# Performance work log

Measured on AMD Instinct MI355X. Metric: run time of the kernel, lower is better.

The kernel has to match this reference:

```python
import jax, jax.numpy as jnp
import numpy as np


def gcn_conv(x, src, dst, W, b, N):
    """PyG GCNConv: add self-loops, symmetric D^-1/2 (A+I) D^-1/2 normalization."""
    loop = jnp.arange(N, dtype=src.dtype)
    s = jnp.concatenate([src, loop])
    d = jnp.concatenate([dst, loop])
    deg = jnp.zeros((N,), dtype=x.dtype).at[d].add(1.0)  # in-degree incl. self-loop
    dinv = jax.lax.rsqrt(deg)  # deg >= 1 because of self-loops
    norm = dinv[s] * dinv[d]  # [E+N]
    h = x @ W  # [N, out] linear transform first (as in PyG)
    msg = h[s] * norm[:, None]  # gather + scale
    out = jax.ops.segment_sum(msg, d, num_segments=N)  # scatter-add
    return out + b


def setup_inputs() -> dict:
    key = jax.random.key(0)
    ks = jax.random.split(key, 10)
    N, E, in_dim, h1, h2, A = 100000, 3200000, 256, 32, 64, 64
    x = jax.random.normal(ks[0], (N, in_dim), dtype=jnp.float32)
    ei = jax.random.randint(ks[1], (2, E), 0, N, dtype=jnp.int64)
    def glorot(k, shape):
        lim = float(np.sqrt(6.0 / (shape[0] + shape[1])))
        return jax.random.uniform(k, shape, jnp.float32, -lim, lim)
    return {
        "x": x,
        "ei": ei,
        "num_nodes": N,
        "W1": glorot(ks[2], (in_dim, h1)), "b1": jnp.zeros((h1,), jnp.float32),
        "W2": glorot(ks[3], (h1, h2)),     "b2": jnp.zeros((h2,), jnp.float32),
        "Wo1": glorot(ks[4], (h2, h2)),    "bo1": jnp.zeros((h2,), jnp.float32),
        "Wo2": glorot(ks[5], (h2, A)),     "bo2": jnp.zeros((A,), jnp.float32),
    }


def reference(x, ei, num_nodes, W1, b1, W2, b2, Wo1, bo1, Wo2, bo2):
    src, dst = ei[0], ei[1]
    z = jax.nn.relu(gcn_conv(x, src, dst, W1, b1, num_nodes))
    z = jax.nn.relu(gcn_conv(z, src, dst, W2, b2, num_nodes))
    logits = jax.nn.relu(z @ Wo1 + bo1) @ Wo2 + bo2  # [N, action_space]
    nbatches = z.shape[0] // num_nodes
    # original reshapes with z.size(1)=hidden2 (== action_space here)
    dist = logits.reshape(nbatches, num_nodes * z.shape[1])
    return jax.nn.softmax(dist, axis=-1)  # Categorical probs
```

## Files before the change

kernel.cpp:

```cpp
#include <hip/hip_runtime.h>

#define DEVI __device__ __forceinline__

DEVI unsigned fkey(float f) {
  unsigned u = __float_as_uint(f);
  return u ^ ((u >> 31) ? 0xFFFFFFFFu : 0x80000000u);
}
DEVI float funkey(unsigned k) {
  unsigned b = (k & 0x80000000u) ? (k ^ 0x80000000u) : ~k;
  return __uint_as_float(b);
}
DEVI float f4get(const float4& v, int j) {
  return j == 0 ? v.x : j == 1 ? v.y : j == 2 ? v.z : v.w;
}

constexpr int BSH = 9;
constexpr int BNODES = 1 << BSH;
constexpr int PEPT = 16;
constexpr int PCHUNK = 256 * PEPT;

__global__ void k_binit(int* __restrict__ bcnt) {
  bcnt[threadIdx.x] = 0;
}

__global__ void k_bcount(const int* __restrict__ dst, int* __restrict__ bcnt,
                         int E, int NB) {
  __shared__ int lh[256];
  lh[threadIdx.x] = 0;
  __syncthreads();
  int stride = gridDim.x * 256;
  for (long i = (long)blockIdx.x * 256 + threadIdx.x; i < E; i += stride)
    atomicAdd(&lh[dst[i] >> BSH], 1);
  __syncthreads();
  if (threadIdx.x < NB && lh[threadIdx.x]) atomicAdd(&bcnt[threadIdx.x], lh[threadIdx.x]);
}

__global__ void k_bscan(const int* __restrict__ bcnt, int* __restrict__ bbase,
                        int* __restrict__ bcur, unsigned* __restrict__ scal, int NB) {
  __shared__ int s[256];
  int t = threadIdx.x;
  int v = (t < NB) ? bcnt[t] : 0;
  s[t] = v;
  __syncthreads();
  for (int o = 1; o < 256; o <<= 1) {
    int add = (t >= o) ? s[t - o] : 0;
    __syncthreads();
    s[t] += add;
    __syncthreads();
  }
  int excl = s[t] - v;
  if (t < NB) { bbase[t] = excl; bcur[t] = excl; }
  if (t == 0) { scal[0] = 0u; scal[1] = 0u; }
}

__global__ __launch_bounds__(256)
void k_bpart(const int* __restrict__ src, const int* __restrict__ dst,
             int* __restrict__ bcur, unsigned* __restrict__ epart, int E, int NB) {
  __shared__ int lh[256];
  __shared__ int gbase[256];
  long base = (long)blockIdx.x * PCHUNK;
  lh[threadIdx.x] = 0;
  __syncthreads();
  int ed[PEPT]; int es[PEPT]; unsigned short lpos[PEPT];
#pragma unroll
  for (int j = 0; j < PEPT; j++) {
    long i = base + threadIdx.x + (long)j * 256;
    if (i < E) {
      int d = dst[i];
      es[j] = src[i];
      ed[j] = d;
      lpos[j] = (unsigned short)atomicAdd(&lh[d >> BSH], 1);
    } else {
      ed[j] = -1;
    }
  }
  __syncthreads();
  if (threadIdx.x < NB) {
    int c = lh[threadIdx.x];
    gbase[threadIdx.x] = c ? atomicAdd(&bcur[threadIdx.x], c) : 0;
  }
  __syncthreads();
#pragma unroll
  for (int j = 0; j < PEPT; j++) {
    int d = ed[j];
    if (d >= 0) {
      unsigned p = (unsigned)(gbase[d >> BSH] + (int)lpos[j]);
      epart[p] = ((unsigned)(d & (BNODES - 1)) << 17) | (unsigned)es[j];
    }
  }
}

__global__ __launch_bounds__(256)
void k_fine(const unsigned* __restrict__ epart, const int* __restrict__ bbase,
            const int* __restrict__ bcnt, int* __restrict__ rowptr,
            int* __restrict__ deg, float* __restrict__ dinv,
            int* __restrict__ col, int N) {
  __shared__ int lh[BNODES];
  __shared__ int lexcl[BNODES];
  __shared__ int ssc[256];
  int b = blockIdx.x;
  int base = bbase[b], cnt = bcnt[b];
  int nlo = b << BSH;
  int t = threadIdx.x;
  lh[t] = 0; lh[t + 256] = 0;
  __syncthreads();
  for (int i = t; i < cnt; i += 256) {
    unsigned e = epart[base + i];
    atomicAdd(&lh[e >> 17], 1);
  }
  __syncthreads();
  int a0 = lh[2 * t], a1 = lh[2 * t + 1];
  ssc[t] = a0 + a1;
  __syncthreads();
  for (int o = 1; o < 256; o <<= 1) {
    int add = (t >= o) ? ssc[t - o] : 0;
    __syncthreads();
    ssc[t] += add;
    __syncthreads();
  }
  int excl = ssc[t] - (a0 + a1);
  lexcl[2 * t] = excl;
  lexcl[2 * t + 1] = excl + a0;
  __syncthreads();
#pragma unroll
  for (int k = 0; k < 2; k++) {
    int i = t + k * 256;
    int v = nlo + i;
    if (v < N) {
      int dgv = lh[i];
      deg[v] = dgv;
      rowptr[v] = base + lexcl[i];
      dinv[v] = rsqrtf((float)(dgv + 1));
    }
  }
  __syncthreads();
  lh[2 * t] = lexcl[2 * t];
  lh[2 * t + 1] = lexcl[2 * t + 1];
  __syncthreads();
  for (int i = t; i < cnt; i += 256) {
    unsigned e = epart[base + i];
    int p = atomicAdd(&lh[e >> 17], 1);
    col[base + p] = (int)(e & 0x1FFFFu);
  }
}

__global__ __launch_bounds__(256)
void k_gemm1(const float* __restrict__ in, const float* __restrict__ W,
             const float* __restrict__ dinv, float* __restrict__ out, int N) {
  __shared__ float Wl[256 * 32];
  __shared__ float xb[2][128 * 16];
  const int t = threadIdx.x;

  {
    const float4* W4 = (const float4*)W;
    float4* Wl4 = (float4*)Wl;
#pragma unroll
    for (int i = 0; i < 8; i++) Wl4[t + i * 256] = W4[t + i * 256];
  }

  const int srow = t >> 1;
  const int part = t & 1;
  const int sk = (srow >> 1) & 3;
  long grow = (long)blockIdx.x * 128 + srow;
  const float* gsrc = in + (grow < (long)N ? grow : (long)(N - 1)) * 256 + part * 8;
  const int q0 = part * 2, q1 = part * 2 + 1;
  const int ws0 = srow * 16 + ((q0 ^ sk) << 2);
  const int ws1 = srow * 16 + ((q1 ^ sk) << 2);

  const int cg = t & 3;
  const int rg = t >> 2;
  const int c0 = cg * 8;
  const int rk = (rg >> 1) & 3;

  {
    float4 a = *(const float4*)(gsrc + 0);
    float4 b = *(const float4*)(gsrc + 4);
    *(float4*)&xb[0][ws0] = a;
    *(float4*)&xb[0][ws1] = b;
  }
  __syncthreads();

  float acc[2][8];
#pragma unroll
  for (int i = 0; i < 2; i++)
#pragma unroll
    for (int c = 0; c < 8; c++) acc[i][c] = 0.f;

  for (int ch = 0; ch < 16; ch++) {
    float4 na, nb;
    if (ch < 15) {
      na = *(const float4*)(gsrc + (ch + 1) * 16 + 0);
      nb = *(const float4*)(gsrc + (ch + 1) * 16 + 4);
    }
    const float* xc = xb[ch & 1];
#pragma unroll
    for (int q = 0; q < 4; q++) {
      float4 xv0 = *(const float4*)&xc[rg * 16 + ((q ^ rk) << 2)];
      float4 xv1 = *(const float4*)&xc[(rg + 64) * 16 + ((q ^ rk) << 2)];
#pragma unroll
      for (int jj = 0; jj < 4; jj++) {
        const float* wr = &Wl[(ch * 16 + q * 4 + jj) * 32 + c0];
        float4 wa = *(const float4*)(wr);
        float4 wb = *(const float4*)(wr + 4);
        float x0 = f4get(xv0, jj);
        float x1 = f4get(xv1, jj);
        acc[0][0] = fmaf(x0, wa.x, acc[0][0]);
        acc[0][1] = fmaf(x0, wa.y, acc[0][1]);
        acc[0][2] = fmaf(x0, wa.z, acc[0][2]);
        acc[0][3] = fmaf(x0, wa.w, acc[0][3]);
        acc[0][4] = fmaf(x0, wb.x, acc[0][4]);
        acc[0][5] = fmaf(x0, wb.y, acc[0][5]);
        acc[0][6] = fmaf(x0, wb.z, acc[0][6]);
        acc[0][7] = fmaf(x0, wb.w, acc[0][7]);
        acc[1][0] = fmaf(x1, wa.x, acc[1][0]);
        acc[1][1] = fmaf(x1, wa.y, acc[1][1]);
        acc[1][2] = fmaf(x1, wa.z, acc[1][2]);
        acc[1][3] = fmaf(x1, wa.w, acc[1][3]);
        acc[1][4] = fmaf(x1, wb.x, acc[1][4]);
        acc[1][5] = fmaf(x1, wb.y, acc[1][5]);
        acc[1][6] = fmaf(x1, wb.z, acc[1][6]);
        acc[1][7] = fmaf(x1, wb.w, acc[1][7]);
      }
    }
    if (ch < 15) {
      __syncthreads();
      float* xn = xb[(ch + 1) & 1];
      *(float4*)&xn[ws0] = na;
      *(float4*)&xn[ws1] = nb;
      __syncthreads();
    }
  }

#pragma unroll
  for (int i = 0; i < 2; i++) {
    long r = (long)blockIdx.x * 128 + rg + i * 64;
    if (r < (long)N) {
      float dv = dinv[r];
      float* op = &out[r * 32 + c0];
      *(float4*)(op) = make_float4(acc[i][0] * dv, acc[i][1] * dv,
                                   acc[i][2] * dv, acc[i][3] * dv);
      *(float4*)(op + 4) = make_float4(acc[i][4] * dv, acc[i][5] * dv,
                                       acc[i][6] * dv, acc[i][7] * dv);
    }
  }
}

__global__ __launch_bounds__(256)
void k_head(const float* __restrict__ s2,
            const float* __restrict__ W2, const float* __restrict__ b2,
            const float* __restrict__ Wo1, const float* __restrict__ bo1,
            const float* __restrict__ Wo2, const float* __restrict__ bo2,
            float* __restrict__ out, int N, unsigned* __restrict__ gmax) {
  __shared__ float A[64 * 64];
  __shared__ float B[64 * 64];
  __shared__ float xr[128 * 64];
  const int t = threadIdx.x;
  const int cg = t & 7, rg = t >> 3;
  const int c0 = cg * 8;
  const int key = rg & 7;
  const long r0 = (long)blockIdx.x * 128 + rg * 4;

  {
    const float4* w2 = (const float4*)W2;
    const float4* w1 = (const float4*)Wo1;
    float4* Af = (float4*)A;
    float4* Bf = (float4*)B;
    Af[t] = w2[t];
    Af[t + 256] = w2[t + 256];
#pragma unroll
    for (int i = 0; i < 4; i++) Bf[t + i * 256] = w1[t + i * 256];
  }
  __syncthreads();

  bool rv[4];
  int xrow[4];
#pragma unroll
  for (int i = 0; i < 4; i++) {
    rv[i] = (r0 + i) < (long)N;
    xrow[i] = (rg + 32 * i) * 64;
  }

  float acc[4][8];

#pragma unroll
  for (int i = 0; i < 4; i++)
#pragma unroll
    for (int c = 0; c < 8; c++) acc[i][c] = 0.f;
  {
    const float* ip = s2 + r0 * 32;
#pragma unroll 2
    for (int k = 0; k < 32; k += 4) {
      float4 xv[4];
#pragma unroll
      for (int i = 0; i < 4; i++)
        xv[i] = rv[i] ? *(const float4*)(ip + i * 32 + k)
                      : make_float4(0.f, 0.f, 0.f, 0.f);
#pragma unroll
      for (int jj = 0; jj < 4; jj++) {
        float4 wa = *(const float4*)&A[(k + jj) * 64 + c0];
        float4 wb = *(const float4*)&A[(k + jj) * 64 + c0 + 4];
#pragma unroll
        for (int i = 0; i < 4; i++) {
          float xs = f4get(xv[i], jj);
          acc[i][0] = fmaf(xs, wa.x, acc[i][0]);
          acc[i][1] = fmaf(xs, wa.y, acc[i][1]);
          acc[i][2] = fmaf(xs, wa.z, acc[i][2]);
          acc[i][3] = fmaf(xs, wa.w, acc[i][3]);
          acc[i][4] = fmaf(xs, wb.x, acc[i][4]);
          acc[i][5] = fmaf(xs, wb.y, acc[i][5]);
          acc[i][6] = fmaf(xs, wb.z, acc[i][6]);
          acc[i][7] = fmaf(xs, wb.w, acc[i][7]);
        }
      }
    }
    float bo[8];
#pragma unroll
    for (int c = 0; c < 8; c++) bo[c] = b2[c0 + c];
    const int q0 = (2 * cg) ^ key, q1 = (2 * cg + 1) ^ key;
#pragma unroll
    for (int i = 0; i < 4; i++) {
      float v0 = fmaxf(acc[i][0] + bo[0], 0.f);
      float v1 = fmaxf(acc[i][1] + bo[1], 0.f);
      float v2 = fmaxf(acc[i][2] + bo[2], 0.f);
      float v3 = fmaxf(acc[i][3] + bo[3], 0.f);
      float v4 = fmaxf(acc[i][4] + bo[4], 0.f);
      float v5 = fmaxf(acc[i][5] + bo[5], 0.f);
      float v6 = fmaxf(acc[i][6] + bo[6], 0.f);
      float v7 = fmaxf(acc[i][7] + bo[7], 0.f);
      *(float4*)&xr[xrow[i] + 4 * q0] = make_float4(v0, v1, v2, v3);
      *(float4*)&xr[xrow[i] + 4 * q1] = make_float4(v4, v5, v6, v7);
    }
  }
  __syncthreads();

  float4 wo2r[4];
  {
    const float4* w = (const float4*)Wo2;
#pragma unroll
    for (int i = 0; i < 4; i++) wo2r[i] = w[t + i * 256];
  }

#pragma unroll
  for (int i = 0; i < 4; i++)
#pragma unroll
    for (int c = 0; c < 8; c++) acc[i][c] = 0.f;
#pragma unroll 2
  for (int k = 0; k < 64; k += 4) {
    const int q = k >> 2;
    float4 xv[4];
#pragma unroll
    for (int i = 0; i < 4; i++)
      xv[i] = *(const float4*)&xr[xrow[i] + 4 * (q ^ key)];
#pragma unroll
    for (int jj = 0; jj < 4; jj++) {
      float4 wa = *(const float4*)&B[(k + jj) * 64 + c0];
      float4 wb = *(const float4*)&B[(k + jj) * 64 + c0 + 4];
#pragma unroll
      for (int i = 0; i < 4; i++) {
        float xs = f4get(xv[i], jj);
        acc[i][0] = fmaf(xs, wa.x, acc[i][0]);
        acc[i][1] = fmaf(xs, wa.y, acc[i][1]);
        acc[i][2] = fmaf(xs, wa.z, acc[i][2]);
        acc[i][3] = fmaf(xs, wa.w, acc[i][3]);
        acc[i][4] = fmaf(xs, wb.x, acc[i][4]);
        acc[i][5] = fmaf(xs, wb.y, acc[i][5]);
        acc[i][6] = fmaf(xs, wb.z, acc[i][6]);
        acc[i][7] = fmaf(xs, wb.w, acc[i][7]);
      }
    }
  }
  __syncthreads();

  {
    float4* Af = (float4*)A;
#pragma unroll
    for (int i = 0; i < 4; i++) Af[t + i * 256] = wo2r[i];
    float bo[8];
#pragma unroll
    for (int c = 0; c < 8; c++) bo[c] = bo1[c0 + c];
    const int q0 = (2 * cg) ^ key, q1 = (2 * cg + 1) ^ key;
#pragma unroll
    for (int i = 0; i < 4; i++) {
      float v0 = fmaxf(acc[i][0] + bo[0], 0.f);
      float v1 = fmaxf(acc[i][1] + bo[1], 0.f);
      float v2 = fmaxf(acc[i][2] + bo[2], 0.f);
      float v3 = fmaxf(acc[i][3] + bo[3], 0.f);
      float v4 = fmaxf(acc[i][4] + bo[4], 0.f);
      float v5 = fmaxf(acc[i][5] + bo[5], 0.f);
      float v6 = fmaxf(acc[i][6] + bo[6], 0.f);
      float v7 = fmaxf(acc[i][7] + bo[7], 0.f);
      *(float4*)&xr[xrow[i] + 4 * q0] = make_float4(v0, v1, v2, v3);
      *(float4*)&xr[xrow[i] + 4 * q1] = make_float4(v4, v5, v6, v7);
    }
  }
  __syncthreads();

#pragma unroll
  for (int i = 0; i < 4; i++)
#pragma unroll
    for (int c = 0; c < 8; c++) acc[i][c] = 0.f;
#pragma unroll 2
  for (int k = 0; k < 64; k += 4) {
    const int q = k >> 2;
    float4 xv[4];
#pragma unroll
    for (int i = 0; i < 4; i++)
      xv[i] = *(const float4*)&xr[xrow[i] + 4 * (q ^ key)];
#pragma unroll
    for (int jj = 0; jj < 4; jj++) {
      float4 wa = *(const float4*)&A[(k + jj) * 64 + c0];
      float4 wb = *(const float4*)&A[(k + jj) * 64 + c0 + 4];
#pragma unroll
      for (int i = 0; i < 4; i++) {
        float xs = f4get(xv[i], jj);
        acc[i][0] = fmaf(xs, wa.x, acc[i][0]);
        acc[i][1] = fmaf(xs, wa.y, acc[i][1]);
        acc[i][2] = fmaf(xs, wa.z, acc[i][2]);
        acc[i][3] = fmaf(xs, wa.w, acc[i][3]);
        acc[i][4] = fmaf(xs, wb.x, acc[i][4]);
        acc[i][5] = fmaf(xs, wb.y, acc[i][5]);
        acc[i][6] = fmaf(xs, wb.z, acc[i][6]);
        acc[i][7] = fmaf(xs, wb.w, acc[i][7]);
      }
    }
  }
  float m = -3.4e38f;
  {
    float bo[8];
#pragma unroll
    for (int c = 0; c < 8; c++) bo[c] = bo2[c0 + c];
#pragma unroll
    for (int i = 0; i < 4; i++) {
      if (!rv[i]) continue;
      float o[8];
#pragma unroll
      for (int c = 0; c < 8; c++) {
        float v = acc[i][c] + bo[c];
        m = fmaxf(m, v);
        o[c] = v;
      }
      float* op = &out[(r0 + i) * 64 + c0];
      *(float4*)(op) = make_float4(o[0], o[1], o[2], o[3]);
      *(float4*)(op + 4) = make_float4(o[4], o[5], o[6], o[7]);
    }
  }
  __syncthreads();
  xr[t] = m;
  __syncthreads();
  for (int o2 = 128; o2 > 0; o2 >>= 1) {
    if (t < o2) xr[t] = fmaxf(xr[t], xr[t + o2]);
    __syncthreads();
  }
  if (t == 0) atomicMax(gmax, fkey(xr[0]));
}

template <int FEAT, bool BIAS, bool RELU, bool PSCALE>
__launch_bounds__(256)
__global__ void k_aggv(const float* __restrict__ g, const int* __restrict__ col,
                       const int* __restrict__ rowptr, const int* __restrict__ deg,
                       const float* __restrict__ dinv, const float* __restrict__ bias,
                       float* __restrict__ out, int N) {
  constexpr int LPN = FEAT / 4;
  constexpr int NPB = 256 / LPN;
  int nib = threadIdx.x / LPN;
  int c = threadIdx.x % LPN;
  long v = (long)blockIdx.x * NPB + nib;
  if (v >= N) return;

  const float4* g4 = (const float4*)g;
  float4 acc = g4[v * LPN + c];
  int start = rowptr[v], dg = deg[v];
  int e = 0;
  while (e < dg) {
    int cnt = min(LPN, dg - e);
    int idx = (c < cnt) ? col[start + e + c] : 0;
    int j = 0;
    for (; j + 4 <= cnt; j += 4) {
      int u0 = __shfl(idx, j + 0, LPN);
      int u1 = __shfl(idx, j + 1, LPN);
      int u2 = __shfl(idx, j + 2, LPN);
      int u3 = __shfl(idx, j + 3, LPN);
      float4 a0 = g4[(long)u0 * LPN + c];
      float4 a1 = g4[(long)u1 * LPN + c];
      float4 a2 = g4[(long)u2 * LPN + c];
      float4 a3 = g4[(long)u3 * LPN + c];
      acc.x += (a0.x + a1.x) + (a2.x + a3.x);
      acc.y += (a0.y + a1.y) + (a2.y + a3.y);
      acc.z += (a0.z + a1.z) + (a2.z + a3.z);
      acc.w += (a0.w + a1.w) + (a2.w + a3.w);
    }
    for (; j < cnt; j++) {
      int u = __shfl(idx, j, LPN);
      float4 a = g4[(long)u * LPN + c];
      acc.x += a.x; acc.y += a.y; acc.z += a.z; acc.w += a.w;
    }
    e += cnt;
  }
  float dv = dinv[v];
  float4 val;
  val.x = acc.x * dv; val.y = acc.y * dv; val.z = acc.z * dv; val.w = acc.w * dv;
  if (BIAS) {
    float4 b = ((const float4*)bias)[c];
    val.x += b.x; val.y += b.y; val.z += b.z; val.w += b.w;
  }
  if (RELU) {
    val.x = fmaxf(val.x, 0.f); val.y = fmaxf(val.y, 0.f);
    val.z = fmaxf(val.z, 0.f); val.w = fmaxf(val.w, 0.f);
  }
  if (PSCALE) {
    val.x *= dv; val.y *= dv; val.z *= dv; val.w *= dv;
  }
  ((float4*)out)[v * LPN + c] = val;
}

__global__ void k_smsum(const float* __restrict__ logit, unsigned* __restrict__ scal, int total) {
  __shared__ float s[256];
  float gmax = funkey(scal[0]);
  float loc = 0.f;
  for (int i = blockIdx.x * 256 + threadIdx.x; i < total; i += gridDim.x * 256)
    loc += expf(logit[i] - gmax);
  s[threadIdx.x] = loc; __syncthreads();
  for (int o = 128; o > 0; o >>= 1) {
    if (threadIdx.x < o) s[threadIdx.x] += s[threadIdx.x + o];
    __syncthreads();
  }
  if (threadIdx.x == 0) atomicAdd((float*)&scal[1], s[0]);
}

__global__ void k_smnorm(float* __restrict__ logit, const unsigned* __restrict__ scal, int total) {
  float gmax = funkey(scal[0]);
  float inv = 1.0f / __uint_as_float(scal[1]);
  int i = blockIdx.x * 256 + threadIdx.x;
  if (i < total) logit[i] = expf(logit[i] - gmax) * inv;
}

extern "C" void kernel_launch(void* const* d_in, const int* in_sizes, int n_in,
                              void* d_out, int out_size, void* d_ws, size_t ws_size,
                              hipStream_t stream) {
  const float* x   = (const float*)d_in[0];
  const int*   ei  = (const int*)d_in[1];
  const float* W1  = (const float*)d_in[3];
  const float* b1  = (const float*)d_in[4];
  const float* W2  = (const float*)d_in[5];
  const float* b2  = (const float*)d_in[6];
  const float* Wo1 = (const float*)d_in[7];
  const float* bo1 = (const float*)d_in[8];
  const float* Wo2 = (const float*)d_in[9];
  const float* bo2 = (const float*)d_in[10];

  const int N = in_sizes[0] / 256;
  const int E = in_sizes[1] / 2;
  const int* src = ei;
  const int* dst = ei + E;
  const int NB = (N + BNODES - 1) / BNODES;

  size_t o = 0;
  auto carve = [&](size_t bytes) -> char* {
    char* p = (char*)d_ws + o;
    o += (bytes + 255) & ~(size_t)255;
    return p;
  };
  float* R1     = (float*)carve((size_t)N * 64 * 4);
  float* R2     = (float*)carve((size_t)N * 64 * 4);
  int*   col    = (int*)carve((size_t)E * 4);
  int*   deg    = (int*)carve((size_t)N * 4);
  float* dinv   = (float*)carve((size_t)N * 4);
  int*   rowptr = (int*)carve((size_t)N * 4);
  int*   bcnt   = (int*)carve(256 * 4);
  int*   bbase  = (int*)carve(256 * 4);
  int*   bcur   = (int*)carve(256 * 4);
  unsigned* scal = (unsigned*)carve(64);

  unsigned* epart = (unsigned*)R2;
  float* g1 = R1;
  float* p  = R2;
  float* s2 = R1;
  float* logits = (float*)d_out;

  k_binit<<<1, 256, 0, stream>>>(bcnt);
  k_bcount<<<512, 256, 0, stream>>>(dst, bcnt, E, NB);
  k_bscan<<<1, 256, 0, stream>>>(bcnt, bbase, bcur, scal, NB);
  k_bpart<<<(E + PCHUNK - 1) / PCHUNK, 256, 0, stream>>>(src, dst, bcur, epart, E, NB);
  k_fine<<<NB, 256, 0, stream>>>(epart, bbase, bcnt, rowptr, deg, dinv, col, N);

  const int g1G = (N + 127) / 128;
  const int gA = (N + 31) / 32;

  k_gemm1<<<g1G, 256, 0, stream>>>(x, W1, dinv, g1, N);
  k_aggv<32, true, true, true><<<gA, 256, 0, stream>>>(g1, col, rowptr, deg, dinv, b1, p, N);

  k_aggv<32, false, false, false><<<gA, 256, 0, stream>>>(p, col, rowptr, deg, dinv, nullptr, s2, N);

  k_head<<<g1G, 256, 0, stream>>>(s2, W2, b2, Wo1, bo1, Wo2, bo2, logits, N, scal);

  k_smsum<<<1024, 256, 0, stream>>>(logits, scal, out_size);
  k_smnorm<<<(out_size + 255) / 256, 256, 0, stream>>>(logits, scal, out_size);
}
```

Baseline: 495.9 us.

## Keep head MLP activations in registers and exchange via shuffles instead of LDS

The fused head kernel no longer stages intermediate activations through a large shared-memory tile. Each group of 8 lanes exchanges its row's activation values with width-8 shuffles, and only one 16KB weight buffer is kept, reloaded between layers. The block max reduction becomes a wavefront shuffle reduction with one atomic per wave rather than a tree over shared memory. This cuts LDS use sharply, which should allow more resident blocks, at the cost of many extra shuffle instructions and more register pressure.

```diff
diff --git a/kernel.cpp b/kernel.cpp
--- a/kernel.cpp
+++ b/kernel.cpp
@@ -252,40 +252,35 @@
             const float* __restrict__ Wo2, const float* __restrict__ bo2,
             float* __restrict__ out, int N, unsigned* __restrict__ gmax) {
   __shared__ float A[64 * 64];
-  __shared__ float B[64 * 64];
-  __shared__ float xr[128 * 64];
   const int t = threadIdx.x;
   const int cg = t & 7, rg = t >> 3;
   const int c0 = cg * 8;
-  const int key = rg & 7;
   const long r0 = (long)blockIdx.x * 128 + rg * 4;
 
   {
     const float4* w2 = (const float4*)W2;
-    const float4* w1 = (const float4*)Wo1;
     float4* Af = (float4*)A;
-    float4* Bf = (float4*)B;
     Af[t] = w2[t];
     Af[t + 256] = w2[t + 256];
-#pragma unroll
-    for (int i = 0; i < 4; i++) Bf[t + i * 256] = w1[t + i * 256];
+  }
+  float4 wn[4];
+  {
+    const float4* w = (const float4*)Wo1;
+#pragma unroll
+    for (int i = 0; i < 4; i++) wn[i] = w[t + i * 256];
   }
   __syncthreads();
 
   bool rv[4];
-  int xrow[4];
-#pragma unroll
-  for (int i = 0; i < 4; i++) {
-    rv[i] = (r0 + i) < (long)N;
-    xrow[i] = (rg + 32 * i) * 64;
-  }
-
-  float acc[4][8];
+#pragma unroll
+  for (int i = 0; i < 4; i++) rv[i] = (r0 + i) < (long)N;
+
+  float a1[4][8], a2[4][8];
 
 #pragma unroll
   for (int i = 0; i < 4; i++)
 #pragma unroll
-    for (int c = 0; c < 8; c++) acc[i][c] = 0.f;
+    for (int c = 0; c < 8; c++) a1[i][c] = 0.f;
   {
     const float* ip = s2 + r0 * 32;
 #pragma unroll 2
@@ -302,128 +297,122 @@
 #pragma unroll
         for (int i = 0; i < 4; i++) {
           float xs = f4get(xv[i], jj);
-          acc[i][0] = fmaf(xs, wa.x, acc[i][0]);
-          acc[i][1] = fmaf(xs, wa.y, acc[i][1]);
-          acc[i][2] = fmaf(xs, wa.z, acc[i][2]);
-          acc[i][3] = fmaf(xs, wa.w, acc[i][3]);
-          acc[i][4] = fmaf(xs, wb.x, acc[i][4]);
-          acc[i][5] = fmaf(xs, wb.y, acc[i][5]);
-          acc[i][6] = fmaf(xs, wb.z, acc[i][6]);
-          acc[i][7] = fmaf(xs, wb.w, acc[i][7]);
+          a1[i][0] = fmaf(xs, wa.x, a1[i][0]);
+          a1[i][1] = fmaf(xs, wa.y, a1[i][1]);
+          a1[i][2] = fmaf(xs, wa.z, a1[i][2]);
+          a1[i][3] = fmaf(xs, wa.w, a1[i][3]);
+          a1[i][4] = fmaf(xs, wb.x, a1[i][4]);
+          a1[i][5] = fmaf(xs, wb.y, a1[i][5]);
+          a1[i][6] = fmaf(xs, wb.z, a1[i][6]);
+          a1[i][7] = fmaf(xs, wb.w, a1[i][7]);
         }
       }
     }
     float bo[8];
 #pragma unroll
     for (int c = 0; c < 8; c++) bo[c] = b2[c0 + c];
-    const int q0 = (2 * cg) ^ key, q1 = (2 * cg + 1) ^ key;
-#pragma unroll
-    for (int i = 0; i < 4; i++) {
-      float v0 = fmaxf(acc[i][0] + bo[0], 0.f);
-      float v1 = fmaxf(acc[i][1] + bo[1], 0.f);
-      float v2 = fmaxf(acc[i][2] + bo[2], 0.f);
-      float v3 = fmaxf(acc[i][3] + bo[3], 0.f);
-      float v4 = fmaxf(acc[i][4] + bo[4], 0.f);
-      float v5 = fmaxf(acc[i][5] + bo[5], 0.f);
-      float v6 = fmaxf(acc[i][6] + bo[6], 0.f);
-      float v7 = fmaxf(acc[i][7] + bo[7], 0.f);
-      *(float4*)&xr[xrow[i] + 4 * q0] = make_float4(v0, v1, v2, v3);
-      *(float4*)&xr[xrow[i] + 4 * q1] = make_float4(v4, v5, v6, v7);
-    }
-  }
-  __syncthreads();
-
-  float4 wo2r[4];
-  {
+#pragma unroll
+    for (int i = 0; i < 4; i++)
+#pragma unroll
+      for (int c = 0; c < 8; c++) a1[i][c] = fmaxf(a1[i][c] + bo[c], 0.f);
+  }
+
+  __syncthreads();
+  {
+    float4* Af = (float4*)A;
+#pragma unroll
+    for (int i = 0; i < 4; i++) Af[t + i * 256] = wn[i];
     const float4* w = (const float4*)Wo2;
 #pragma unroll
-    for (int i = 0; i < 4; i++) wo2r[i] = w[t + i * 256];
-  }
+    for (int i = 0; i < 4; i++) wn[i] = w[t + i * 256];
+  }
+  __syncthreads();
 
 #pragma unroll
   for (int i = 0; i < 4; i++)
 #pragma unroll
-    for (int c = 0; c < 8; c++) acc[i][c] = 0.f;
+    for (int c = 0; c < 8; c++) a2[i][c] = 0.f;
 #pragma unroll 2
-  for (int k = 0; k < 64; k += 4) {
-    const int q = k >> 2;
-    float4 xv[4];
+  for (int s = 0; s < 8; s++) {
+    const float* wr = &A[(s * 8) * 64 + c0];
+#pragma unroll
+    for (int e = 0; e < 8; e++) {
+      float4 wa = *(const float4*)(wr + e * 64);
+      float4 wb = *(const float4*)(wr + e * 64 + 4);
+      float x0 = __shfl(a1[0][e], s, 8);
+      float x1 = __shfl(a1[1][e], s, 8);
+      float x2 = __shfl(a1[2][e], s, 8);
+      float x3 = __shfl(a1[3][e], s, 8);
+      a2[0][0] = fmaf(x0, wa.x, a2[0][0]); a2[0][1] = fmaf(x0, wa.y, a2[0][1]);
+      a2[0][2] = fmaf(x0, wa.z, a2[0][2]); a2[0][3] = fmaf(x0, wa.w, a2[0][3]);
+      a2[0][4] = fmaf(x0, wb.x, a2[0][4]); a2[0][5] = fmaf(x0, wb.y, a2[0][5]);
+      a2[0][6] = fmaf(x0, wb.z, a2[0][6]); a2[0][7] = fmaf(x0, wb.w, a2[0][7]);
+      a2[1][0] = fmaf(x1, wa.x, a2[1][0]); a2[1][1] = fmaf(x1, wa.y, a2[1][1]);
+      a2[1][2] = fmaf(x1, wa.z, a2[1][2]); a2[1][3] = fmaf(x1, wa.w, a2[1][3]);
+      a2[1][4] = fmaf(x1, wb.x, a2[1][4]); a2[1][5] = fmaf(x1, wb.y, a2[1][5]);
+      a2[1][6] = fmaf(x1, wb.z, a2[1][6]); a2[1][7] = fmaf(x1, wb.w, a2[1][7]);
+      a2[2][0] = fmaf(x2, wa.x, a2[2][0]); a2[2][1] = fmaf(x2, wa.y, a2[2][1]);
+      a2[2][2] = fmaf(x2, wa.z, a2[2][2]); a2[2][3] = fmaf(x2, wa.w, a2[2][3]);
+      a2[2][4] = fmaf(x2, wb.x, a2[2][4]); a2[2][5] = fmaf(x2, wb.y, a2[2][5]);
+      a2[2][6] = fmaf(x2, wb.z, a2[2][6]); a2[2][7] = fmaf(x2, wb.w, a2[2][7]);
+      a2[3][0] = fmaf(x3, wa.x, a2[3][0]); a2[3][1] = fmaf(x3, wa.y, a2[3][1]);
+      a2[3][2] = fmaf(x3, wa.z, a2[3][2]); a2[3][3] = fmaf(x3, wa.w, a2[3][3]);
+      a2[3][4] = fmaf(x3, wb.x, a2[3][4]); a2[3][5] = fmaf(x3, wb.y, a2[3][5]);
+      a2[3][6] = fmaf(x3, wb.z, a2[3][6]); a2[3][7] = fmaf(x3, wb.w, a2[3][7]);
+    }
+  }
+  {
+    float bo[8];
+#pragma unroll
+    for (int c = 0; c < 8; c++) bo[c] = bo1[c0 + c];
 #pragma unroll
     for (int i = 0; i < 4; i++)
-      xv[i] = *(const float4*)&xr[xrow[i] + 4 * (q ^ key)];
-#pragma unroll
-    for (int jj = 0; jj < 4; jj++) {
-      float4 wa = *(const float4*)&B[(k + jj) * 64 + c0];
-      float4 wb = *(const float4*)&B[(k + jj) * 64 + c0 + 4];
-#pragma unroll
-      for (int i = 0; i < 4; i++) {
-        float xs = f4get(xv[i], jj);
-        acc[i][0] = fmaf(xs, wa.x, acc[i][0]);
-        acc[i][1] = fmaf(xs, wa.y, acc[i][1]);
-        acc[i][2] = fmaf(xs, wa.z, acc[i][2]);
-        acc[i][3] = fmaf(xs, wa.w, acc[i][3]);
-        acc[i][4] = fmaf(xs, wb.x, acc[i][4]);
-        acc[i][5] = fmaf(xs, wb.y, acc[i][5]);
-        acc[i][6] = fmaf(xs, wb.z, acc[i][6]);
-        acc[i][7] = fmaf(xs, wb.w, acc[i][7]);
-      }
-    }
-  }
-  __syncthreads();
-
+#pragma unroll
+      for (int c = 0; c < 8; c++) a2[i][c] = fmaxf(a2[i][c] + bo[c], 0.f);
+  }
+
+  __syncthreads();
   {
     float4* Af = (float4*)A;
 #pragma unroll
-    for (int i = 0; i < 4; i++) Af[t + i * 256] = wo2r[i];
-    float bo[8];
-#pragma unroll
-    for (int c = 0; c < 8; c++) bo[c] = bo1[c0 + c];
-    const int q0 = (2 * cg) ^ key, q1 = (2 * cg + 1) ^ key;
-#pragma unroll
-    for (int i = 0; i < 4; i++) {
-      float v0 = fmaxf(acc[i][0] + bo[0], 0.f);
-      float v1 = fmaxf(acc[i][1] + bo[1], 0.f);
-      float v2 = fmaxf(acc[i][2] + bo[2], 0.f);
-      float v3 = fmaxf(acc[i][3] + bo[3], 0.f);
-      float v4 = fmaxf(acc[i][4] + bo[4], 0.f);
-      float v5 = fmaxf(acc[i][5] + bo[5], 0.f);
-      float v6 = fmaxf(acc[i][6] + bo[6], 0.f);
-      float v7 = fmaxf(acc[i][7] + bo[7], 0.f);
-      *(float4*)&xr[xrow[i] + 4 * q0] = make_float4(v0, v1, v2, v3);
-      *(float4*)&xr[xrow[i] + 4 * q1] = make_float4(v4, v5, v6, v7);
-    }
+    for (int i = 0; i < 4; i++) Af[t + i * 256] = wn[i];
   }
   __syncthreads();
 
 #pragma unroll
   for (int i = 0; i < 4; i++)
 #pragma unroll
-    for (int c = 0; c < 8; c++) acc[i][c] = 0.f;
+    for (int c = 0; c < 8; c++) a1[i][c] = 0.f;
 #pragma unroll 2
-  for (int k = 0; k < 64; k += 4) {
-    const int q = k >> 2;
-    float4 xv[4];
-#pragma unroll
-    for (int i = 0; i < 4; i++)
-      xv[i] = *(const float4*)&xr[xrow[i] + 4 * (q ^ key)];
-#pragma unroll
-    for (int jj = 0; jj < 4; jj++) {
-      float4 wa = *(const float4*)&A[(k + jj) * 64 + c0];
-      float4 wb = *(const float4*)&A[(k + jj) * 64 + c0 + 4];
-#pragma unroll
-      for (int i = 0; i < 4; i++) {
-        float xs = f4get(xv[i], jj);
-        acc[i][0] = fmaf(xs, wa.x, acc[i][0]);
-        acc[i][1] = fmaf(xs, wa.y, acc[i][1]);
-        acc[i][2] = fmaf(xs, wa.z, acc[i][2]);
-        acc[i][3] = fmaf(xs, wa.w, acc[i][3]);
-        acc[i][4] = fmaf(xs, wb.x, acc[i][4]);
-        acc[i][5] = fmaf(xs, wb.y, acc[i][5]);
-        acc[i][6] = fmaf(xs, wb.z, acc[i][6]);
-        acc[i][7] = fmaf(xs, wb.w, acc[i][7]);
-      }
-    }
-  }
+  for (int s = 0; s < 8; s++) {
+    const float* wr = &A[(s * 8) * 64 + c0];
+#pragma unroll
+    for (int e = 0; e < 8; e++) {
+      float4 wa = *(const float4*)(wr + e * 64);
+      float4 wb = *(const float4*)(wr + e * 64 + 4);
+      float x0 = __shfl(a2[0][e], s, 8);
+      float x1 = __shfl(a2[1][e], s, 8);
+      float x2 = __shfl(a2[2][e], s, 8);
+      float x3 = __shfl(a2[3][e], s, 8);
+      a1[0][0] = fmaf(x0, wa.x, a1[0][0]); a1[0][1] = fmaf(x0, wa.y, a1[0][1]);
+      a1[0][2] = fmaf(x0, wa.z, a1[0][2]); a1[0][3] = fmaf(x0, wa.w, a1[0][3]);
+      a1[0][4] = fmaf(x0, wb.x, a1[0][4]); a1[0][5] = fmaf(x0, wb.y, a1[0][5]);
+      a1[0][6] = fmaf(x0, wb.z, a1[0][6]); a1[0][7] = fmaf(x0, wb.w, a1[0][7]);
+      a1[1][0] = fmaf(x1, wa.x, a1[1][0]); a1[1][1] = fmaf(x1, wa.y, a1[1][1]);
+      a1[1][2] = fmaf(x1, wa.z, a1[1][2]); a1[1][3] = fmaf(x1, wa.w, a1[1][3]);
+      a1[1][4] = fmaf(x1, wb.x, a1[1][4]); a1[1][5] = fmaf(x1, wb.y, a1[1][5]);
+      a1[1][6] = fmaf(x1, wb.z, a1[1][6]); a1[1][7] = fmaf(x1, wb.w, a1[1][7]);
+      a1[2][0] = fmaf(x2, wa.x, a1[2][0]); a1[2][1] = fmaf(x2, wa.y, a1[2][1]);
+      a1[2][2] = fmaf(x2, wa.z, a1[2][2]); a1[2][3] = fmaf(x2, wa.w, a1[2][3]);
+      a1[2][4] = fmaf(x2, wb.x, a1[2][4]); a1[2][5] = fmaf(x2, wb.y, a1[2][5]);
+      a1[2][6] = fmaf(x2, wb.z, a1[2][6]); a1[2][7] = fmaf(x2, wb.w, a1[2][7]);
+      a1[3][0] = fmaf(x3, wa.x, a1[3][0]); a1[3][1] = fmaf(x3, wa.y, a1[3][1]);
+      a1[3][2] = fmaf(x3, wa.z, a1[3][2]); a1[3][3] = fmaf(x3, wa.w, a1[3][3]);
+      a1[3][4] = fmaf(x3, wb.x, a1[3][4]); a1[3][5] = fmaf(x3, wb.y, a1[3][5]);
+      a1[3][6] = fmaf(x3, wb.z, a1[3][6]); a1[3][7] = fmaf(x3, wb.w, a1[3][7]);
+    }
+  }
+
   float m = -3.4e38f;
   {
     float bo[8];
@@ -435,7 +424,7 @@
       float o[8];
 #pragma unroll
       for (int c = 0; c < 8; c++) {
-        float v = acc[i][c] + bo[c];
+        float v = a1[i][c] + bo[c];
         m = fmaxf(m, v);
         o[c] = v;
       }
@@ -444,14 +433,9 @@
       *(float4*)(op + 4) = make_float4(o[4], o[5], o[6], o[7]);
     }
   }
-  __syncthreads();
-  xr[t] = m;
-  __syncthreads();
-  for (int o2 = 128; o2 > 0; o2 >>= 1) {
-    if (t < o2) xr[t] = fmaxf(xr[t], xr[t + o2]);
-    __syncthreads();
-  }
-  if (t == 0) atomicMax(gmax, fkey(xr[0]));
+#pragma unroll
+  for (int o2 = 1; o2 < 64; o2 <<= 1) m = fmaxf(m, __shfl_xor(m, o2, 64));
+  if ((t & 63) == 0) atomicMax(gmax, fkey(m));
 }
 
 template <int FEAT, bool BIAS, bool RELU, bool PSCALE>
```

New measurement: 516.9 us. +4.2%, slower.
